# Kernel optimization log

Hardware: AMD Instinct MI355X
Metric: run time of the kernel (lower is better)

Reference implementation:

```python
import jax, jax.numpy as jnp
import numpy as np
from jax import lax

B, C_G, H, W = 2, 64, 240, 1216
NUM, K, IDX_REF = 8, 9, 4  # prop_kernel=3
PROP_TIME = 6


def conv3x3(x, w, b):
    y = lax.conv_general_dilated(x, w, (1, 1), ((1, 1), (1, 1)),
                                 dimension_numbers=('NCHW', 'OIHW', 'NCHW'))
    return y + b[None, :, None, None]


def bilinear_sample(img, y, x):
    """img: (B,H,W); y,x: (B,K,H,W) absolute coords; zero padding outside."""
    Hh, Ww = img.shape[1], img.shape[2]
    y0 = jnp.floor(y)
    x0 = jnp.floor(x)
    wy1, wx1 = y - y0, x - x0
    gather = jax.vmap(lambda im, a, b: im[a, b])
    out = jnp.zeros_like(y)
    for i, (yy, wy) in enumerate(((y0, 1.0 - wy1), (y0 + 1.0, wy1))):
        for j, (xx, wx) in enumerate(((x0, 1.0 - wx1), (x0 + 1.0, wx1))):
            valid = (yy >= 0) & (yy <= Hh - 1) & (xx >= 0) & (xx <= Ww - 1)
            yi = jnp.clip(yy, 0, Hh - 1).astype(jnp.int32)
            xi = jnp.clip(xx, 0, Ww - 1).astype(jnp.int32)
            v = gather(img, yi, xi)
            out = out + wy * wx * jnp.where(valid, v, 0.0)
    return out


def setup_inputs() -> dict:
    key = jax.random.key(0)
    ks = jax.random.split(key, 6)
    return {
        'initial_disp': jax.random.uniform(ks[0], (B, 1, H, W), jnp.float32) * 50.0,
        'occlus_mask': jax.random.uniform(ks[1], (B, 1, H, W), jnp.float32),
        'confidence': jax.random.uniform(ks[2], (B, 1, H, W), jnp.float32),
        'guidance_feature': jax.random.normal(ks[3], (B, C_G, H, W), jnp.float32),
        'conv_w': 0.05 * jax.random.normal(ks[4], (3 * NUM, C_G, 3, 3), jnp.float32),
        'conv_b': jnp.zeros((3 * NUM,), jnp.float32),
        'aff_scale_const': jnp.full((1,), 0.5 * NUM, jnp.float32),  # TGASS: gamma*num
    }


def nlspn_forward(initial_disp, occlus_mask, confidence, guidance_feature,
                  conv_w, conv_b, aff_scale_const):
    Bb, _, Hh, Ww = guidance_feature.shape
    oa = conv3x3(guidance_feature, conv_w, conv_b)          # (B, 3*num, H, W)
    o1, o2, aff = oa[:, :NUM], oa[:, NUM:2 * NUM], oa[:, 2 * NUM:]
    off = jnp.concatenate([o1, o2], axis=1).reshape(Bb, NUM, 2, Hh, Ww)
    zero = jnp.zeros((Bb, 1, 2, Hh, Ww), off.dtype)
    off = jnp.concatenate([off[:, :IDX_REF], zero, off[:, IDX_REF:]], axis=1)  # (B,9,2,H,W)

    # TGASS affinity
    aff = jnp.tanh(aff) / (aff_scale_const[0] + 1e-8)       # (B,8,H,W)

    gy = jnp.arange(Hh, dtype=jnp.float32)[None, None, :, None]
    gx = jnp.arange(Ww, dtype=jnp.float32)[None, None, None, :]

    # confidence sampling: 1x1 deform conv (w_conf=1, bias=0), detached offsets
    off_sg = lax.stop_gradient(off)
    nb = jnp.array([0, 1, 2, 3, 5, 6, 7, 8])
    conf_s = bilinear_sample(confidence[:, 0],
                             gy + off_sg[:, nb, 0], gx + off_sg[:, nb, 1])  # (B,8,H,W)
    aff = aff * conf_s

    s = jnp.sum(jnp.abs(aff), axis=1, keepdims=True) + 1e-5
    s = jnp.where(s < 1.0, 1.0, s)
    aff = aff / s
    aff_ref = 1.0 - jnp.sum(aff, axis=1, keepdims=True)
    aff_full = jnp.concatenate([aff[:, :IDX_REF], aff_ref, aff[:, IDX_REF:]], axis=1)  # (B,9,H,W)

    # 3x3 deform conv grid (stride 1, pad 1, dil 1), weight=ones, bias=0
    kh = (jnp.arange(K) // 3 - 1).astype(jnp.float32).reshape(1, K, 1, 1)
    kw = (jnp.arange(K) % 3 - 1).astype(jnp.float32).reshape(1, K, 1, 1)
    sy = gy + kh + off[:, :, 0]
    sx = gx + kw + off[:, :, 1]

    disp = initial_disp
    list_disp = []
    for _ in range(PROP_TIME):
        samp = bilinear_sample(disp[:, 0], sy, sx)           # (B,9,H,W)
        disp = jnp.sum(aff_full * samp, axis=1, keepdims=True)
        disp = jnp.maximum(disp, 0.0)
        disp = (1.0 - occlus_mask) * disp + occlus_mask * initial_disp
        list_disp.append(disp)
    disp = jnp.maximum(disp, 0.0)

    offset_flat = off.reshape(Bb, 2 * K, Hh, Ww)
    return disp, jnp.stack(list_disp), offset_flat, aff_full, aff_scale_const


def reference(initial_disp, occlus_mask, confidence, guidance_feature,
              conv_w, conv_b, aff_scale_const):
    return nlspn_forward(initial_disp, occlus_mask, confidence, guidance_feature,
                         conv_w, conv_b, aff_scale_const)
```

## Files before the change

### kernel.cpp

```cpp
#include <hip/hip_runtime.h>
#include <hip/hip_bf16.h>
#include <math.h>
#include <string.h>

typedef __attribute__((ext_vector_type(8))) short bf16x8;
typedef __attribute__((ext_vector_type(4))) float f32x4;

constexpr int Bc = 2, CGc = 64, Hc = 240, Wc = 1216;
constexpr int IDXR = 4, PROP = 6;
constexpr long HW  = (long)Hc * Wc;
constexpr long BHW = (long)Bc * HW;

constexpr long OUT0 = 0;
constexpr long OUT1 = BHW;
constexpr long OUT2 = BHW * 7;
constexpr long OUT3 = OUT2 + (long)Bc * 18 * HW;
constexpr long OUT4 = OUT3 + (long)Bc * 9 * HW;

constexpr int HP = Hc + 2, WPAD = Wc + 2;
constexpr long APXB   = (long)HP * WPAD;
constexpr long A_TOT  = (long)Bc * APXB * 128;
constexpr long WOFF   = A_TOT;
constexpr int  W_STRIDE_TAP = 24 * 128;
constexpr long WS_NEED = WOFF + 27648 + 5120;

constexpr int PR = 4, PC = 64, HLO = 6;
constexpr int TR = PR + 2 * HLO;
constexpr int TC = PC + 2 * HLO + 1;

__device__ __forceinline__ unsigned short f2bf(float f) {
  __hip_bfloat16 h = __float2bfloat16(f);
  return __builtin_bit_cast(unsigned short, h);
}
__device__ __forceinline__ unsigned short f2h(float f) {
  _Float16 h = (_Float16)f;
  return __builtin_bit_cast(unsigned short, h);
}
__device__ __forceinline__ float h2f(unsigned short u) {
  return (float)__builtin_bit_cast(_Float16, u);
}
__device__ __forceinline__ float fast_tanh(float x) {
  float xc = fminf(fmaxf(x, -15.f), 15.f);
  float e = __expf(2.f * xc);
  return (e - 1.f) / (e + 1.f);
}

__device__ __forceinline__ void row2(const float* __restrict__ img, int yy, int x0,
                                     float& a, float& b) {
  if (yy >= 0 && yy < Hc) {
    if (x0 >= 0 && x0 < Wc - 1) {
      float2 v;
      __builtin_memcpy(&v, img + (long)yy * Wc + x0, 8);
      a = v.x; b = v.y;
    } else {
      a = (x0 >= 0 && x0 < Wc)         ? img[(long)yy * Wc + x0]     : 0.f;
      b = (x0 + 1 >= 0 && x0 + 1 < Wc) ? img[(long)yy * Wc + x0 + 1] : 0.f;
    }
  } else { a = 0.f; b = 0.f; }
}

__device__ __forceinline__ float bilin(const float* __restrict__ img, float y, float x) {
  float y0f = floorf(y), x0f = floorf(x);
  int y0 = (int)y0f, x0 = (int)x0f;
  float wy = y - y0f, wx = x - x0f;
  float v00, v01, v10, v11;
  row2(img, y0,     x0, v00, v01);
  row2(img, y0 + 1, x0, v10, v11);
  float top = v00 + wx * (v01 - v00);
  float bot = v10 + wx * (v11 - v10);
  return top + wy * (bot - top);
}

__device__ __forceinline__ float bilin_tile(
    const float (*tile)[TC], const float* __restrict__ db,
    int y0, int x0, float sy, float sx) {
  float yf = floorf(sy), xf = floorf(sx);
  int iy = (int)yf, ix = (int)xf;
  float wy = sy - yf, wx = sx - xf;
  if (iy >= y0 - HLO && iy + 1 <= y0 + PR - 1 + HLO &&
      ix >= x0 - HLO && ix + 1 <= x0 + PC - 1 + HLO) {
    int ly = iy - (y0 - HLO), lx = ix - (x0 - HLO);
    float v00 = tile[ly][lx],     v01 = tile[ly][lx + 1];
    float v10 = tile[ly + 1][lx], v11 = tile[ly + 1][lx + 1];
    float top = v00 + wx * (v01 - v00);
    float bot = v10 + wx * (v11 - v10);
    return top + wy * (bot - top);
  }
  return bilin(db, sy, sx);
}

__device__ __forceinline__ void stage_tile(
    float (*tile)[TC], const float* __restrict__ db, int y0, int x0, int tid) {
  for (int i = tid; i < TR * TC; i += 256) {
    int rr = i / TC, cc = i - rr * TC;
    int gy = y0 - HLO + rr, gx = x0 - HLO + cc;
    tile[rr][cc] = (gy >= 0 && gy < Hc && gx >= 0 && gx < Wc)
                       ? db[(long)gy * Wc + gx] : 0.f;
  }
}

__global__ __launch_bounds__(256) void nhwc_kernel(
    const float* __restrict__ g, char* __restrict__ ws) {
  __shared__ __align__(16) char tileb[64 * 132];
  const int tid = threadIdx.x;
  const int x0 = blockIdx.x * 64;
  const int y  = blockIdx.y;
  const int bz = blockIdx.z;
  const float* gb = g + (long)bz * CGc * HW + (long)y * Wc + x0;
  const int px = tid & 63, wv = tid >> 6;
#pragma unroll
  for (int k = 0; k < 16; ++k) {
    int ic = k * 4 + wv;
    float v = gb[(long)ic * HW + px];
    *reinterpret_cast<unsigned short*>(tileb + px * 132 + ic * 2) = f2bf(v);
  }
  __syncthreads();
  const int opx = tid >> 2, q = tid & 3;
  unsigned int u[8];
#pragma unroll
  for (int j = 0; j < 8; ++j)
    u[j] = *reinterpret_cast<unsigned int*>(tileb + opx * 132 + q * 32 + j * 4);
  char* dst = ws + ((long)(bz * HP + y + 1) * WPAD + x0 + 1 + opx) * 128 + q * 32;
  reinterpret_cast<uint4*>(dst)[0] = make_uint4(u[0], u[1], u[2], u[3]);
  reinterpret_cast<uint4*>(dst)[1] = make_uint4(u[4], u[5], u[6], u[7]);
}

__global__ __launch_bounds__(256) void border_kernel(char* __restrict__ ws) {
  constexpr int NB = 2 * WPAD + 2 * (HP - 2);
  long i = (long)blockIdx.x * 256 + threadIdx.x;
  if (i >= (long)Bc * NB) return;
  int bz = (int)(i / NB);
  int r  = (int)(i - (long)bz * NB);
  int py, px;
  if (r < WPAD)            { py = 0;      px = r; }
  else if (r < 2 * WPAD)   { py = HP - 1; px = r - WPAD; }
  else { int qq = r - 2 * WPAD; py = 1 + (qq >> 1); px = (qq & 1) ? (WPAD - 1) : 0; }
  char* p = ws + ((long)(bz * HP + py) * WPAD + px) * 128;
  uint4 z = make_uint4(0, 0, 0, 0);
#pragma unroll
  for (int j = 0; j < 8; ++j) reinterpret_cast<uint4*>(p)[j] = z;
}

__global__ __launch_bounds__(256) void wconv_kernel(
    const float* __restrict__ w, char* __restrict__ ws) {
  char* wd = ws + WOFF;
  int idx = blockIdx.x * 256 + threadIdx.x;
  if (idx < 24 * 64 * 9) {
    int oc = idx / 576, r = idx - oc * 576;
    int ic = r / 9, tap = r - ic * 9;
    *reinterpret_cast<unsigned short*>(wd + tap * W_STRIDE_TAP + oc * 128 + ic * 2) = f2bf(w[idx]);
  } else if (idx < 24 * 64 * 9 + 2560) {
    int i2 = idx - 24 * 64 * 9;
    *reinterpret_cast<unsigned short*>(wd + 27648 + i2 * 2) = 0;
  }
}

constexpr int CTILE_BYTES = 6 * 66 * 128;
constexpr int CUNITS = CTILE_BYTES / 16;
constexpr int EXST = 33;
constexpr int EXCH_BYTES = 4 * 64 * EXST * 4;
constexpr int DT_OFF = EXCH_BYTES;
constexpr int CT_OFF = DT_OFF + TR * TC * 4;
constexpr int TILE_N = TR * TC;

__global__ __launch_bounds__(256) void conv_fused_kernel(
    const char* __restrict__ ws, const float* __restrict__ bias,
    const float* __restrict__ conf, const float* __restrict__ scale_p,
    const float* __restrict__ occm, const float* __restrict__ initd,
    float* __restrict__ out) {
  __shared__ __align__(16) char smemA[CTILE_BYTES];
  const int tid  = threadIdx.x;
  const int lane = tid & 63, wv = tid >> 6;
  const int lrow = lane & 15, lgrp = lane >> 4;
  const int x0 = blockIdx.x * 64;
  const int y0 = blockIdx.y * 4;
  const int bz = blockIdx.z;

  const char* Abase = ws + ((long)(bz * HP + y0) * WPAD + x0) * 128;
#pragma unroll
  for (int it = 0; it < 13; ++it) {
    int u = it * 256 + tid;
    if (u < CUNITS) {
      int pxl = u >> 3, j = u & 7;
      int r = pxl / 66, col = pxl - r * 66;
      uint4 v = *reinterpret_cast<const uint4*>(
          Abase + ((long)r * WPAD + col) * 128 + j * 16);
      int ldsb = pxl * 128 + ((j ^ (col & 7)) << 4);
      *reinterpret_cast<uint4*>(smemA + ldsb) = v;
    }
  }

  const float* db    = initd + (long)bz * HW;
  const float* confb = conf  + (long)bz * HW;
  float rD[5], rC[5];
#pragma unroll
  for (int k = 0; k < 5; ++k) {
    int i = k * 256 + tid;
    rD[k] = 0.f; rC[k] = 0.f;
    if (i < TILE_N) {
      int rr = i / TC, cc = i - rr * TC;
      int gy = y0 - HLO + rr, gx = x0 - HLO + cc;
      if (gy >= 0 && gy < Hc && gx >= 0 && gx < Wc) {
        long o = (long)gy * Wc + gx;
        rD[k] = db[o];
        rC[k] = confb[o];
      }
    }
  }
  __syncthreads();

  const char* Wb = ws + WOFF + (long)lrow * 128 + lgrp * 16;

  f32x4 acc[4][2];
#pragma unroll
  for (int h = 0; h < 4; ++h)
#pragma unroll
    for (int nt = 0; nt < 2; ++nt) acc[h][nt] = (f32x4){0.f, 0.f, 0.f, 0.f};

#pragma unroll
  for (int tap = 0; tap < 9; ++tap) {
    const int dy = tap / 3, dx = tap - dy * 3;
    const char* Wt = Wb + tap * W_STRIDE_TAP;
#pragma unroll
    for (int ks = 0; ks < 2; ++ks) {
      bf16x8 wf0 = *reinterpret_cast<const bf16x8*>(Wt + ks * 64);
      bf16x8 wf1 = *reinterpret_cast<const bf16x8*>(Wt + 2048 + ks * 64);
#pragma unroll
      for (int h = 0; h < 4; ++h) {
        const int colc = lrow + dx + h * 16;
        int abyte = ((wv + dy) * 66 + colc) * 128 +
                    ((((ks << 2) + lgrp) ^ (colc & 7)) << 4);
        bf16x8 af = *reinterpret_cast<const bf16x8*>(smemA + abyte);
        acc[h][0] = __builtin_amdgcn_mfma_f32_16x16x32_bf16(af, wf0, acc[h][0], 0, 0, 0);
        acc[h][1] = __builtin_amdgcn_mfma_f32_16x16x32_bf16(af, wf1, acc[h][1], 0, 0, 0);
      }
    }
  }
  __syncthreads();

  float* exch = reinterpret_cast<float*>(smemA);
  float* dflat = reinterpret_cast<float*>(smemA + DT_OFF);
  float* cflat = reinterpret_cast<float*>(smemA + CT_OFF);
  {
    const int y = y0 + wv;
#pragma unroll
    for (int h = 0; h < 4; ++h) {
      const int xx = x0 + h * 16 + lgrp * 4;
      const int lpx = h * 16 + lgrp * 4;
#pragma unroll
      for (int nt = 0; nt < 2; ++nt) {
        int oc = nt * 16 + lrow;
        if (oc >= 24) continue;
        float bv = bias[oc];
        f32x4 v = acc[h][nt];
#pragma unroll
        for (int j = 0; j < 4; ++j)
          exch[(wv * 64 + lpx + j) * EXST + oc] = v[j] + bv;
        if (oc < 16) {
          int n = oc >> 1, cd = oc & 1;
          int mm = (n < IDXR) ? n : n + 1;
          long dst = OUT2 + (long)(bz * 18 + 2 * mm + cd) * HW;
          float4 st = make_float4(v[0] + bv, v[1] + bv, v[2] + bv, v[3] + bv);
          *reinterpret_cast<float4*>(&out[dst + (long)y * Wc + xx]) = st;
        }
      }
    }
  }
#pragma unroll
  for (int k = 0; k < 5; ++k) {
    int i = k * 256 + tid;
    if (i < TILE_N) { dflat[i] = rD[k]; cflat[i] = rC[k]; }
  }
  __syncthreads();

  float (*dtile)[TC] = reinterpret_cast<float (*)[TC]>(smemA + DT_OFF);
  float (*ctile)[TC] = reinterpret_cast<float (*)[TC]>(smemA + CT_OFF);
  const int row = tid >> 6, px = tid & 63;
  const int y = y0 + row, x = x0 + px;
  long rem = (long)y * Wc + x;
  long p = (long)bz * HW + rem;

  float ch[24];
#pragma unroll
  for (int j = 0; j < 24; ++j) ch[j] = exch[(row * 64 + px) * EXST + j];

  const float inv_scale = 1.f / (scale_p[0] + 1e-8f);
  float* off  = out + OUT2 + (long)bz * 18 * HW + rem;
  float* affp = out + OUT3 + (long)bz * 9  * HW + rem;

  float affr[9], oyr[9], oxr[9];
  float asum = 0.f;
#pragma unroll
  for (int m = 0; m < 8; m++) {
    int n = (m < IDXR) ? m : m + 1;
    float oy  = ch[2 * m];
    float ox  = ch[2 * m + 1];
    float raw = ch[16 + m];
    float avv = fast_tanh(raw) * inv_scale;
    float cs  = bilin_tile(ctile, confb, y0, x0, (float)y + oy, (float)x + ox);
    affr[n] = avv * cs;
    oyr[n] = oy; oxr[n] = ox;
    asum += fabsf(affr[n]);
  }
  float s = fmaxf(asum + 1e-5f, 1.0f);
  float inv_s = 1.f / s;
  float total = 0.f;
#pragma unroll
  for (int m = 0; m < 8; m++) {
    int n = (m < IDXR) ? m : m + 1;
    affr[n] *= inv_s; total += affr[n];
  }
  affr[IDXR] = 1.f - total;
  oyr[IDXR] = 0.f; oxr[IDXR] = 0.f;
#pragma unroll
  for (int n = 0; n < 9; n++) affp[(long)n * HW] = affr[n];
  off[(long)(2 * IDXR) * HW]     = 0.f;
  off[(long)(2 * IDXR + 1) * HW] = 0.f;
  if (p == 0) out[OUT4] = scale_p[0];

  float occv  = occm[p];
  float initv = dtile[HLO + row][HLO + px];
  float acc0 = 0.f;
#pragma unroll
  for (int k = 0; k < 9; k++) {
    float sy = (float)(y + k / 3 - 1) + oyr[k];
    float sx = (float)(x + k % 3 - 1) + oxr[k];
    acc0 = fmaf(affr[k], bilin_tile(dtile, db, y0, x0, sy, sx), acc0);
  }
  acc0 = fmaxf(acc0, 0.f);
  out[OUT1 + p] = (1.f - occv) * acc0 + occv * initv;
}

__global__ __launch_bounds__(256) void prop_tab1_kernel(
    const float* __restrict__ dispPrev,
    const float* __restrict__ occ, const float* __restrict__ initd,
    float* __restrict__ out, uint4* __restrict__ tab4) {
  __shared__ float tile[TR][TC];
  const int tid = threadIdx.x;
  const int x0 = blockIdx.x * PC;
  const int y0 = blockIdx.y * PR;
  const int b  = blockIdx.z;
  const float* db = dispPrev + (long)b * HW;
  stage_tile(tile, db, y0, x0, tid);
  __syncthreads();

  const int y = y0 + (tid >> 6);
  const int x = x0 + (tid & 63);
  long rem = (long)y * Wc + x;
  long p = (long)b * HW + rem;

  const float* off  = out + OUT2 + (long)b * 18 * HW + rem;
  const float* affp = out + OUT3 + (long)b * 9  * HW + rem;

  float affv[9], oyv[9], oxv[9];
#pragma unroll
  for (int k = 0; k < 9; k++) {
    oyv[k]  = off[(long)(2 * k) * HW];
    oxv[k]  = off[(long)(2 * k + 1) * HW];
    affv[k] = affp[(long)k * HW];
  }
  float occv  = occ[p];
  float initv = initd[p];

  float acc = 0.f;
#pragma unroll
  for (int k = 0; k < 9; k++) {
    float sy = (float)(y + k / 3 - 1) + oyv[k];
    float sx = (float)(x + k % 3 - 1) + oxv[k];
    acc = fmaf(affv[k], bilin_tile(tile, db, y0, x0, sy, sx), acc);
  }
  acc = fmaxf(acc, 0.f);
  float res = (1.f - occv) * acc + occv * initv;
  out[OUT1 + (long)1 * BHW + p] = res;

  unsigned short hs[28];
#pragma unroll
  for (int k = 0; k < 9; k++) {
    hs[k] = f2h(affv[k]); hs[9 + k] = f2h(oyv[k]); hs[18 + k] = f2h(oxv[k]);
  }
  hs[27] = 0;
  unsigned u[16];
#pragma unroll
  for (int i = 0; i < 14; i++)
    u[i] = (unsigned)hs[2 * i] | ((unsigned)hs[2 * i + 1] << 16);
  u[14] = __builtin_bit_cast(unsigned, occv);
  u[15] = __builtin_bit_cast(unsigned, initv);
#pragma unroll
  for (int g = 0; g < 4; g++)
    tab4[(long)g * BHW + p] = make_uint4(u[4 * g], u[4 * g + 1], u[4 * g + 2], u[4 * g + 3]);
}

__global__ __launch_bounds__(256) void prop_tabN_kernel(
    const float* __restrict__ dispPrev, const uint4* __restrict__ tab4,
    float* __restrict__ out, int t) {
  __shared__ float tile[TR][TC];
  const int tid = threadIdx.x;
  const int x0 = blockIdx.x * PC;
  const int y0 = blockIdx.y * PR;
  const int b  = blockIdx.z;
  const float* db = dispPrev + (long)b * HW;
  stage_tile(tile, db, y0, x0, tid);
  __syncthreads();

  const int y = y0 + (tid >> 6);
  const int x = x0 + (tid & 63);
  long rem = (long)y * Wc + x;
  long p = (long)b * HW + rem;

  unsigned u[16];
#pragma unroll
  for (int g = 0; g < 4; g++) {
    uint4 q = tab4[(long)g * BHW + p];
    u[4 * g] = q.x; u[4 * g + 1] = q.y; u[4 * g + 2] = q.z; u[4 * g + 3] = q.w;
  }
  float fl[27];
#pragma unroll
  for (int i = 0; i < 27; i++) {
    unsigned w0 = u[i >> 1];
    fl[i] = h2f((unsigned short)((i & 1) ? (w0 >> 16) : (w0 & 0xffff)));
  }
  float occv  = __builtin_bit_cast(float, u[14]);
  float initv = __builtin_bit_cast(float, u[15]);

  float acc = 0.f;
#pragma unroll
  for (int k = 0; k < 9; k++) {
    float sy = (float)(y + k / 3 - 1) + fl[9 + k];
    float sx = (float)(x + k % 3 - 1) + fl[18 + k];
    acc = fmaf(fl[k], bilin_tile(tile, db, y0, x0, sy, sx), acc);
  }
  acc = fmaxf(acc, 0.f);
  float res = (1.f - occv) * acc + occv * initv;
  out[OUT1 + (long)t * BHW + p] = res;
  if (t == PROP - 1) out[OUT0 + p] = res;
}

constexpr int TY = 8, TX = 32;
constexpr int AR = TY + 2, AC = TX + 2;
constexpr int A_BYTES = AR * AC * CGc * 2;
constexpr int W_BYTES = 9 * 32 * 32 * 2;

__global__ __launch_bounds__(256) void conv_mfma_kernel(
    const float* __restrict__ g, const float* __restrict__ wsrc,
    const float* __restrict__ bias, float* __restrict__ out) {
  __shared__ __align__(16) char smemA[A_BYTES];
  __shared__ __align__(16) char smemW[W_BYTES];
  const int tid = threadIdx.x;
  const int x0 = blockIdx.x * TX;
  const int y0 = blockIdx.y * TY;
  const int bz = blockIdx.z;
  const float* gb = g + (long)bz * CGc * HW;
  for (int w = tid; w < AR * AC * 32; w += 256) {
    int c  = w % AC;
    int t2 = w / AC;
    int icp = t2 & 31;
    int r   = t2 >> 5;
    int y = y0 + r - 1, x = x0 + c - 1;
    float v0 = 0.f, v1 = 0.f;
    if (y >= 0 && y < Hc && x >= 0 && x < Wc) {
      const float* p = gb + (long)(2 * icp) * HW + (long)y * Wc + x;
      v0 = p[0]; v1 = p[HW];
    }
    unsigned int pk = (unsigned int)f2bf(v0) | ((unsigned int)f2bf(v1) << 16);
    int byte = (r * AC + c) * 128 + icp * 4;
    byte ^= (c & 7) << 4;
    *reinterpret_cast<unsigned int*>(smemA + byte) = pk;
  }
  auto stageW = [&](int hs) {
    for (int idx = tid; idx < 24 * 32 * 9; idx += 256) {
      int oc  = idx / 288;
      int r1  = idx - oc * 288;
      int icl = r1 / 9;
      int tap = r1 - icl * 9;
      float f = wsrc[idx + 288 * (oc + hs)];
      int byte = (tap * 32 + oc) * 64 + icl * 2;
      byte ^= (oc & 7) << 4;
      *reinterpret_cast<unsigned short*>(smemW + byte) = f2bf(f);
    }
  };
  stageW(0);
  __syncthreads();
  const int wid  = tid >> 6;
  const int lane = tid & 63;
  const int lrow = lane & 15;
  const int lgrp = lane >> 4;
  f32x4 acc[4][2];
#pragma unroll
  for (int m = 0; m < 4; m++)
#pragma unroll
    for (int nt = 0; nt < 2; nt++) acc[m][nt] = (f32x4){0.f, 0.f, 0.f, 0.f};
  for (int ks = 0; ks < 2; ++ks) {
    if (ks) { __syncthreads(); stageW(1); __syncthreads(); }
#pragma unroll
    for (int tap = 0; tap < 9; ++tap) {
      const int dy = tap / 3, dx = tap - dy * 3;
      int bb = (tap * 32 + lrow) * 64 + lgrp * 16;
      int bbyte0 = bb ^ ((lrow & 7) << 4);
      int bbyte1 = (bb + 16 * 64) ^ ((lrow & 7) << 4);
      bf16x8 bf0 = *reinterpret_cast<const bf16x8*>(smemW + bbyte0);
      bf16x8 bf1 = *reinterpret_cast<const bf16x8*>(smemW + bbyte1);
#pragma unroll
      for (int dr = 0; dr < 2; ++dr) {
        const int rin = 2 * wid + dr + dy;
#pragma unroll
        for (int h = 0; h < 2; ++h) {
          const int cin = h * 16 + lrow + dx;
          int abyte = ((rin * AC + cin) * 128 + ks * 64 + lgrp * 16) ^ ((cin & 7) << 4);
          bf16x8 af = *reinterpret_cast<const bf16x8*>(smemA + abyte);
          acc[dr * 2 + h][0] = __builtin_amdgcn_mfma_f32_16x16x32_bf16(af, bf0, acc[dr * 2 + h][0], 0, 0, 0);
          acc[dr * 2 + h][1] = __builtin_amdgcn_mfma_f32_16x16x32_bf16(af, bf1, acc[dr * 2 + h][1], 0, 0, 0);
        }
      }
    }
  }
#pragma unroll
  for (int dr = 0; dr < 2; ++dr) {
    const int yy = y0 + 2 * wid + dr;
#pragma unroll
    for (int h = 0; h < 2; ++h) {
      const int xx = x0 + h * 16 + lgrp * 4;
#pragma unroll
      for (int nt = 0; nt < 2; ++nt) {
        int oc = nt * 16 + lrow;
        if (oc >= 24) continue;
        float bv = bias[oc];
        long dst;
        if (oc < 16) {
          int n = oc >> 1, cd = oc & 1;
          int mm = (n < IDXR) ? n : n + 1;
          dst = OUT2 + (long)(bz * 18 + 2 * mm + cd) * HW;
        } else {
          int i2 = oc - 16;
          int mm = (i2 < IDXR) ? i2 : i2 + 1;
          dst = OUT3 + (long)(bz * 9 + mm) * HW;
        }
        f32x4 v = acc[dr * 2 + h][nt];
        float4 st = make_float4(v[0] + bv, v[1] + bv, v[2] + bv, v[3] + bv);
        *reinterpret_cast<float4*>(&out[dst + (long)yy * Wc + xx]) = st;
      }
    }
  }
}

__global__ __launch_bounds__(256) void prep_kernel(
    const float* __restrict__ conf, const float* __restrict__ scale_p,
    float* __restrict__ out) {
  long p = (long)blockIdx.x * 256 + threadIdx.x;
  if (p >= BHW) return;
  int b = (int)(p / HW);
  long rem = p - (long)b * HW;
  int y = (int)(rem / Wc);
  int x = (int)(rem - (long)y * Wc);
  const float inv_scale = 1.f / (scale_p[0] + 1e-8f);
  const float* confb = conf + (long)b * HW;
  float* off  = out + OUT2 + (long)b * 18 * HW + rem;
  float* affp = out + OUT3 + (long)b * 9  * HW + rem;
  float a[8];
  float asum = 0.f;
#pragma unroll
  for (int m = 0; m < 8; m++) {
    int n = (m < IDXR) ? m : m + 1;
    float oy  = off[(long)(2 * n) * HW];
    float ox  = off[(long)(2 * n + 1) * HW];
    float raw = affp[(long)n * HW];
    float av  = tanhf(raw) * inv_scale;
    float cs  = bilin(confb, (float)y + oy, (float)x + ox);
    a[m] = av * cs;
    asum += fabsf(a[m]);
  }
  float s = fmaxf(asum + 1e-5f, 1.0f);
  float inv_s = 1.f / s;
  float total = 0.f;
#pragma unroll
  for (int m = 0; m < 8; m++) { a[m] *= inv_s; total += a[m]; }
  float aref = 1.f - total;
#pragma unroll
  for (int m = 0; m < 8; m++) {
    int n = (m < IDXR) ? m : m + 1;
    affp[(long)n * HW] = a[m];
  }
  affp[(long)IDXR * HW] = aref;
  off[(long)(2 * IDXR) * HW]     = 0.f;
  off[(long)(2 * IDXR + 1) * HW] = 0.f;
  if (p == 0) out[OUT4] = scale_p[0];
}

__global__ __launch_bounds__(256) void prop_kernel(
    const float* __restrict__ dispPrev,
    const float* __restrict__ occ, const float* __restrict__ initd,
    float* __restrict__ out, int t) {
  long p = (long)blockIdx.x * 256 + threadIdx.x;
  if (p >= BHW) return;
  int b = (int)(p / HW);
  long rem = p - (long)b * HW;
  int y = (int)(rem / Wc);
  int x = (int)(rem - (long)y * Wc);
  const float* off  = out + OUT2 + (long)b * 18 * HW + rem;
  const float* affp = out + OUT3 + (long)b * 9  * HW + rem;
  const float* db   = dispPrev + (long)b * HW;
  float acc = 0.f;
#pragma unroll
  for (int k = 0; k < 9; k++) {
    float oy = off[(long)(2 * k) * HW];
    float ox = off[(long)(2 * k + 1) * HW];
    float av = affp[(long)k * HW];
    float sy = (float)(y + k / 3 - 1) + oy;
    float sx = (float)(x + k % 3 - 1) + ox;
    acc = fmaf(av, bilin(db, sy, sx), acc);
  }
  acc = fmaxf(acc, 0.f);
  float o = occ[p];
  float res = (1.f - o) * acc + o * initd[p];
  out[OUT1 + (long)t * BHW + p] = res;
  if (t == PROP - 1) out[OUT0 + p] = res;
}

extern "C" void kernel_launch(void* const* d_in, const int* in_sizes, int n_in,
                              void* d_out, int out_size, void* d_ws, size_t ws_size,
                              hipStream_t stream) {
  const float* initd = (const float*)d_in[0];
  const float* occ   = (const float*)d_in[1];
  const float* conf  = (const float*)d_in[2];
  const float* guid  = (const float*)d_in[3];
  const float* cw    = (const float*)d_in[4];
  const float* cb    = (const float*)d_in[5];
  const float* csc   = (const float*)d_in[6];
  float* out = (float*)d_out;
  int nblk = (int)((BHW + 255) / 256);

  if (ws_size >= (size_t)WS_NEED) {
    char* ws = (char*)d_ws;
    nhwc_kernel<<<dim3(Wc / 64, Hc, Bc), 256, 0, stream>>>(guid, ws);
    border_kernel<<<(Bc * (2 * WPAD + 2 * (HP - 2)) + 255) / 256, 256, 0, stream>>>(ws);
    wconv_kernel<<<72, 256, 0, stream>>>(cw, ws);

    dim3 pgrid(Wc / PC, Hc / PR, Bc);
    conv_fused_kernel<<<pgrid, 256, 0, stream>>>(ws, cb, conf, csc, occ, initd, out);

    uint4* tab4 = (uint4*)ws;
    prop_tab1_kernel<<<pgrid, 256, 0, stream>>>(out + OUT1, occ, initd, out, tab4);
    for (int t = 2; t < PROP; t++) {
      const float* dp = out + OUT1 + (long)(t - 1) * BHW;
      prop_tabN_kernel<<<pgrid, 256, 0, stream>>>(dp, tab4, out, t);
    }
  } else {
    conv_mfma_kernel<<<dim3(Wc / TX, Hc / TY, Bc), 256, 0, stream>>>(guid, cw, cb, out);
    prep_kernel<<<nblk, 256, 0, stream>>>(conf, csc, out);
    for (int t = 0; t < PROP; t++) {
      const float* dp = (t == 0) ? initd : (out + OUT1 + (long)(t - 1) * BHW);
      prop_kernel<<<nblk, 256, 0, stream>>>(dp, occ, initd, out, t);
    }
  }
}
```

Before: 196.8 us.

## Stage conv input channels in two LDS halves and exchange outputs as fp16

The conv tile staging in shared memory is split into two K-halves of 64 bytes per pixel, loaded and consumed in turn, which halves the LDS footprint. The per-pixel channel exchange buffer now stores half-precision values instead of floats, also shrinking LDS. The smaller allocation is meant to allow more resident blocks per CU. In exchange it adds a barrier and a second global load phase, and the offset and affinity values used downstream lose precision because they pass through fp16.

```diff
diff --git a/kernel.cpp b/kernel.cpp
--- a/kernel.cpp
+++ b/kernel.cpp
@@ -155,10 +155,10 @@
   }
 }
 
-constexpr int CTILE_BYTES = 6 * 66 * 128;
-constexpr int CUNITS = CTILE_BYTES / 16;
-constexpr int EXST = 33;
-constexpr int EXCH_BYTES = 4 * 64 * EXST * 4;
+constexpr int STAGE_BYTES = 6 * 66 * 64;
+constexpr int HUNITS = 6 * 66 * 4;
+constexpr int EXST_H = 26;
+constexpr int EXCH_BYTES = 4 * 64 * EXST_H * 2;
 constexpr int DT_OFF = EXCH_BYTES;
 constexpr int CT_OFF = DT_OFF + TR * TC * 4;
 constexpr int TILE_N = TR * TC;
@@ -168,7 +168,7 @@
     const float* __restrict__ conf, const float* __restrict__ scale_p,
     const float* __restrict__ occm, const float* __restrict__ initd,
     float* __restrict__ out) {
-  __shared__ __align__(16) char smemA[CTILE_BYTES];
+  __shared__ __align__(16) char smemA[STAGE_BYTES];
   const int tid  = threadIdx.x;
   const int lane = tid & 63, wv = tid >> 6;
   const int lrow = lane & 15, lgrp = lane >> 4;
@@ -177,18 +177,6 @@
   const int bz = blockIdx.z;
 
   const char* Abase = ws + ((long)(bz * HP + y0) * WPAD + x0) * 128;
-#pragma unroll
-  for (int it = 0; it < 13; ++it) {
-    int u = it * 256 + tid;
-    if (u < CUNITS) {
-      int pxl = u >> 3, j = u & 7;
-      int r = pxl / 66, col = pxl - r * 66;
-      uint4 v = *reinterpret_cast<const uint4*>(
-          Abase + ((long)r * WPAD + col) * 128 + j * 16);
-      int ldsb = pxl * 128 + ((j ^ (col & 7)) << 4);
-      *reinterpret_cast<uint4*>(smemA + ldsb) = v;
-    }
-  }
 
   const float* db    = initd + (long)bz * HW;
   const float* confb = conf  + (long)bz * HW;
@@ -207,7 +195,6 @@
       }
     }
   }
-  __syncthreads();
 
   const char* Wb = ws + WOFF + (long)lrow * 128 + lgrp * 16;
 
@@ -217,19 +204,33 @@
 #pragma unroll
     for (int nt = 0; nt < 2; ++nt) acc[h][nt] = (f32x4){0.f, 0.f, 0.f, 0.f};
 
-#pragma unroll
-  for (int tap = 0; tap < 9; ++tap) {
-    const int dy = tap / 3, dx = tap - dy * 3;
-    const char* Wt = Wb + tap * W_STRIDE_TAP;
-#pragma unroll
-    for (int ks = 0; ks < 2; ++ks) {
+  for (int ks = 0; ks < 2; ++ks) {
+    if (ks) __syncthreads();
+#pragma unroll
+    for (int it = 0; it < 7; ++it) {
+      int u = it * 256 + tid;
+      if (u < HUNITS) {
+        int pxl = u >> 2, j = u & 3;
+        int r = pxl / 66, col = pxl - r * 66;
+        uint4 v = *reinterpret_cast<const uint4*>(
+            Abase + ((long)r * WPAD + col) * 128 + ks * 64 + j * 16);
+        int slot = pxl * 64 + ((j ^ ((col >> 1) & 3)) << 4);
+        *reinterpret_cast<uint4*>(smemA + slot) = v;
+      }
+    }
+    __syncthreads();
+
+#pragma unroll
+    for (int tap = 0; tap < 9; ++tap) {
+      const int dy = tap / 3, dx = tap - dy * 3;
+      const char* Wt = Wb + tap * W_STRIDE_TAP;
       bf16x8 wf0 = *reinterpret_cast<const bf16x8*>(Wt + ks * 64);
       bf16x8 wf1 = *reinterpret_cast<const bf16x8*>(Wt + 2048 + ks * 64);
 #pragma unroll
       for (int h = 0; h < 4; ++h) {
         const int colc = lrow + dx + h * 16;
-        int abyte = ((wv + dy) * 66 + colc) * 128 +
-                    ((((ks << 2) + lgrp) ^ (colc & 7)) << 4);
+        int abyte = ((wv + dy) * 66 + colc) * 64 +
+                    ((lgrp ^ ((colc >> 1) & 3)) << 4);
         bf16x8 af = *reinterpret_cast<const bf16x8*>(smemA + abyte);
         acc[h][0] = __builtin_amdgcn_mfma_f32_16x16x32_bf16(af, wf0, acc[h][0], 0, 0, 0);
         acc[h][1] = __builtin_amdgcn_mfma_f32_16x16x32_bf16(af, wf1, acc[h][1], 0, 0, 0);
@@ -238,7 +239,7 @@
   }
   __syncthreads();
 
-  float* exch = reinterpret_cast<float*>(smemA);
+  unsigned short* exch = reinterpret_cast<unsigned short*>(smemA);
   float* dflat = reinterpret_cast<float*>(smemA + DT_OFF);
   float* cflat = reinterpret_cast<float*>(smemA + CT_OFF);
   {
@@ -255,7 +256,7 @@
         f32x4 v = acc[h][nt];
 #pragma unroll
         for (int j = 0; j < 4; ++j)
-          exch[(wv * 64 + lpx + j) * EXST + oc] = v[j] + bv;
+          exch[(wv * 64 + lpx + j) * EXST_H + oc] = f2h(v[j] + bv);
         if (oc < 16) {
           int n = oc >> 1, cd = oc & 1;
           int mm = (n < IDXR) ? n : n + 1;
@@ -281,8 +282,16 @@
   long p = (long)bz * HW + rem;
 
   float ch[24];
-#pragma unroll
-  for (int j = 0; j < 24; ++j) ch[j] = exch[(row * 64 + px) * EXST + j];
+  {
+    const unsigned* e32 = reinterpret_cast<const unsigned*>(
+        exch + (row * 64 + px) * EXST_H);
+#pragma unroll
+    for (int j = 0; j < 12; ++j) {
+      unsigned w0 = e32[j];
+      ch[2 * j]     = h2f((unsigned short)(w0 & 0xffff));
+      ch[2 * j + 1] = h2f((unsigned short)(w0 >> 16));
+    }
+  }
 
   const float inv_scale = 1.f / (scale_p[0] + 1e-8f);
   float* off  = out + OUT2 + (long)bz * 18 * HW + rem;
```

After: 203.0 us. 3.1% more time.
